# Performance work log

Hardware: AMD Instinct MI355X
Metric: run time of the kernel (lower is better)

The kernel has to match this reference:

```python
import jax, jax.numpy as jnp
import numpy as np

N_NODES = 20000
N_EDGES = 640000
IN_DIM = 256
HID = 128
N_GRAPHS = 64


def setup_inputs() -> dict:
    key = jax.random.key(0)
    ks = jax.random.split(key, 9)
    x = jax.random.normal(ks[0], (N_NODES, IN_DIM), jnp.float32)
    edge_index = jax.random.randint(ks[1], (2, N_EDGES), 0, N_NODES, dtype=jnp.int32)
    batch = jnp.sort(jax.random.randint(ks[2], (N_NODES,), 0, N_GRAPHS, dtype=jnp.int32))

    def lin(k, fan_in, fan_out):
        # torch.nn.Linear default init: U(-1/sqrt(fan_in), 1/sqrt(fan_in))
        bound = 1.0 / np.sqrt(fan_in)
        kw, kb = jax.random.split(k)
        W = jax.random.uniform(kw, (fan_in, fan_out), jnp.float32, -bound, bound)
        b = jax.random.uniform(kb, (fan_out,), jnp.float32, -bound, bound)
        return W, b

    W0, b0 = lin(ks[3], IN_DIM, HID)
    W1, b1 = lin(ks[4], HID, HID)
    W2, b2 = lin(ks[5], HID, HID)
    return dict(x=x, edge_index=edge_index, batch=batch,
                W0=W0, b0=b0, W1=W1, b1=b1, W2=W2, b2=b2)


def reference(x, edge_index, batch, W0, b0, W1, b1, W2, b2):
    src, dst = edge_index[0], edge_index[1]
    edge_batch = batch[src]  # [E] segment id per edge
    ones = jnp.ones((edge_batch.shape[0], 1), x.dtype)
    counts = jax.ops.segment_sum(ones, edge_batch, num_segments=N_GRAPHS)
    inv_counts = 1.0 / jnp.maximum(counts, 1.0)

    def pool(z):
        # gather endpoint features, concat -> [E, 2*HID], mean pool by graph
        edge_emb = jnp.concatenate([z[src], z[dst]], axis=1)
        return jax.ops.segment_sum(edge_emb, edge_batch, num_segments=N_GRAPHS) * inv_counts

    g = []
    z = x
    for W, b in ((W0, b0), (W1, b1), (W2, b2)):
        z = z @ W + b
        g.append(pool(z))
    return jnp.concatenate(g, axis=1)  # [N_GRAPHS, 3 * 2 * HID]
```

## Files before the change

### kernel.cpp

```cpp
#include <hip/hip_runtime.h>

#define N_NODES 20000
#define N_EDGES 640000
#define N_GRAPHS 64

#define NCHUNK 128
#define CHUNK_SZ 157
#define GSPLIT 8
#define GSUB 8

#define BG_TILE 2048
#define NBG 313
#define SEGCAP 80
#define GR_CAP 768
#define NSLOT4 (NBG * SEGCAP / 4)

#define CD_OFF      0
#define DEG_OFF     1280000
#define CNT_OFF     1300000
#define Y_OFF       1300064
#define PART_OFF    1316448
#define BH_OFF      3413600
#define VALS_OFF    3433632

__global__ __launch_bounds__(512) void bucket_g_k(const int* __restrict__ ei,
                                                  const int* __restrict__ batch,
                                                  unsigned* __restrict__ vals,
                                                  unsigned* __restrict__ bh,
                                                  float* __restrict__ Y) {
    __shared__ unsigned hist[N_GRAPHS];
    __shared__ unsigned base[N_GRAPHS + 1];
    __shared__ unsigned lv[BG_TILE];
    __shared__ unsigned char gidx[BG_TILE];
    const int t = threadIdx.x;
    const int blk = blockIdx.x;
    if (t < N_GRAPHS) hist[t] = 0u;
    __syncthreads();

    const int e0 = blk * BG_TILE;
    const int ecnt = (e0 + BG_TILE <= N_EDGES) ? BG_TILE : (N_EDGES - e0);
    unsigned pv[4], rnk[4], gg[4];
#pragma unroll
    for (int k = 0; k < 4; ++k) {
        int i = t + k * 512;
        if (i < ecnt) {
            unsigned s = (unsigned)ei[e0 + i];
            unsigned d = (unsigned)ei[N_EDGES + e0 + i];
            unsigned g = (unsigned)batch[s];
            pv[k] = (s << 15) | d;
            gg[k] = g;
            rnk[k] = atomicAdd(&hist[g], 1u);
        } else {
            gg[k] = 0xFFFFFFFFu;
        }
    }
    __syncthreads();
    if (t < N_GRAPHS) {
        unsigned v = hist[t];
        unsigned sum = v;
#pragma unroll
        for (int off = 1; off < 64; off <<= 1) {
            unsigned u = __shfl_up(sum, off, 64);
            if (t >= off) sum += u;
        }
        base[t + 1] = sum;
        if (t == 0) base[0] = 0u;
        bh[blk * N_GRAPHS + t] = (v > SEGCAP) ? SEGCAP : v;
    }
    __syncthreads();
    if (t < N_GRAPHS) {
        unsigned b0 = base[t], b1 = base[t + 1];
        for (unsigned i = b0; i < b1; ++i) gidx[i] = (unsigned char)t;
    }
#pragma unroll
    for (int k = 0; k < 4; ++k) {
        if (gg[k] != 0xFFFFFFFFu) lv[base[gg[k]] + rnk[k]] = pv[k];
    }
    __syncthreads();
    for (int i = t; i < ecnt; i += 512) {
        unsigned g = gidx[i];
        unsigned slot = (unsigned)i - base[g];
        if (slot < SEGCAP)
            vals[((size_t)g * NBG + blk) * SEGCAP + slot] = lv[i];
    }
    if (blk == 0) {
        float4* y4 = (float4*)Y;
        for (int i = t; i < 64 * 64; i += 512) y4[i] = make_float4(0.f, 0.f, 0.f, 0.f);
    }
}

__global__ __launch_bounds__(1024) void cd_col_k(const unsigned* __restrict__ vals,
                                                 const unsigned* __restrict__ bh,
                                                 const int* __restrict__ batch,
                                                 float* __restrict__ Cdcol,
                                                 float* __restrict__ deg,
                                                 float* __restrict__ counts) {
    __shared__ unsigned scnt[NBG];
    __shared__ unsigned dh[10000];
    __shared__ unsigned sdeg[GR_CAP];
    __shared__ int s_lo, s_hi;
    const int t = threadIdx.x;
    const int g = blockIdx.x;

    for (int i = t; i < 10000; i += 1024) dh[i] = 0u;
    if (t < NBG) scnt[t] = bh[t * N_GRAPHS + g];
    if (t < GR_CAP) sdeg[t] = 0u;
    if (t == 0) {
        int lo = 0, hi = N_NODES;
        while (lo < hi) { int m = (lo + hi) >> 1; if (batch[m] < g) lo = m + 1; else hi = m; }
        s_lo = lo;
        int lo2 = lo; hi = N_NODES;
        while (lo2 < hi) { int m = (lo2 + hi) >> 1; if (batch[m] < g + 1) lo2 = m + 1; else hi = m; }
        s_hi = lo2;
    }
    __syncthreads();
    const int lo = s_lo;

    const uint4* v4 = (const uint4*)(vals + (size_t)g * NBG * SEGCAP);
    for (int i = t; i < NSLOT4; i += 1024) {
        uint4 v = *(v4 + i);
        unsigned w = (unsigned)i * 4u;
        unsigned seg = (unsigned)(((unsigned long long)w * 53687092ull) >> 32);
        unsigned local = w - seg * 80u;
        unsigned c = scnt[seg];
#define CD_ONE(VX, L)                                                            \
        if ((L) < c) {                                                           \
            unsigned rd_ = (VX) & 0x7FFFu;                                       \
            atomicAdd(&dh[rd_ >> 1], 1u << ((rd_ & 1) * 16));                    \
            int rs_ = (int)((VX) >> 15) - lo;                                    \
            if ((unsigned)rs_ < (unsigned)GR_CAP) atomicAdd(&sdeg[rs_], 1u);     \
        }
        CD_ONE(v.x, local + 0u)
        CD_ONE(v.y, local + 1u)
        CD_ONE(v.z, local + 2u)
        CD_ONE(v.w, local + 3u)
#undef CD_ONE
    }
    __syncthreads();

    float2* outc = (float2*)(Cdcol + (size_t)g * N_NODES);
    for (int w = t; w < 10000; w += 1024) {
        unsigned v = dh[w];
        outc[w] = make_float2((float)(v & 0xFFFFu), (float)(v >> 16));
    }
    {
        const int range = s_hi - lo;
        for (int i = t; i < range; i += 1024) deg[lo + i] = (float)sdeg[i];
        if (t == 0) {
            unsigned tot = 0;
            for (int i = 0; i < NBG; ++i) tot += scnt[i];
            counts[g] = (float)tot;
        }
    }
}

#define FMA8(C0, C1, XV)                                          \
    acc[0].x = fmaf(C0.x, XV.x, acc[0].x); acc[0].y = fmaf(C0.x, XV.y, acc[0].y); \
    acc[0].z = fmaf(C0.x, XV.z, acc[0].z); acc[0].w = fmaf(C0.x, XV.w, acc[0].w); \
    acc[1].x = fmaf(C0.y, XV.x, acc[1].x); acc[1].y = fmaf(C0.y, XV.y, acc[1].y); \
    acc[1].z = fmaf(C0.y, XV.z, acc[1].z); acc[1].w = fmaf(C0.y, XV.w, acc[1].w); \
    acc[2].x = fmaf(C0.z, XV.x, acc[2].x); acc[2].y = fmaf(C0.z, XV.y, acc[2].y); \
    acc[2].z = fmaf(C0.z, XV.z, acc[2].z); acc[2].w = fmaf(C0.z, XV.w, acc[2].w); \
    acc[3].x = fmaf(C0.w, XV.x, acc[3].x); acc[3].y = fmaf(C0.w, XV.y, acc[3].y); \
    acc[3].z = fmaf(C0.w, XV.z, acc[3].z); acc[3].w = fmaf(C0.w, XV.w, acc[3].w); \
    acc[4].x = fmaf(C1.x, XV.x, acc[4].x); acc[4].y = fmaf(C1.x, XV.y, acc[4].y); \
    acc[4].z = fmaf(C1.x, XV.z, acc[4].z); acc[4].w = fmaf(C1.x, XV.w, acc[4].w); \
    acc[5].x = fmaf(C1.y, XV.x, acc[5].x); acc[5].y = fmaf(C1.y, XV.y, acc[5].y); \
    acc[5].z = fmaf(C1.y, XV.z, acc[5].z); acc[5].w = fmaf(C1.y, XV.w, acc[5].w); \
    acc[6].x = fmaf(C1.z, XV.x, acc[6].x); acc[6].y = fmaf(C1.z, XV.y, acc[6].y); \
    acc[6].z = fmaf(C1.z, XV.z, acc[6].z); acc[6].w = fmaf(C1.z, XV.w, acc[6].w); \
    acc[7].x = fmaf(C1.w, XV.x, acc[7].x); acc[7].y = fmaf(C1.w, XV.y, acc[7].y); \
    acc[7].z = fmaf(C1.w, XV.z, acc[7].z); acc[7].w = fmaf(C1.w, XV.w, acc[7].w);

__global__ __launch_bounds__(256) void pool_k(const float* __restrict__ x,
                                              const int* __restrict__ batch,
                                              const float* __restrict__ Cdcol,
                                              const float* __restrict__ deg,
                                              float* __restrict__ Y,
                                              float* __restrict__ part) {
    __shared__ float4 sc4[CHUNK_SZ * 2];
    __shared__ float sdeg[CHUNK_SZ];
    __shared__ int   sbatch[CHUNK_SZ];
    __shared__ float4 red[2 * GSUB * 64];

    const int t = threadIdx.x;
    const int fg = t & 63;
    const int p  = t >> 6;
    const int b = blockIdx.x & 127;
    const int j = blockIdx.x >> 7;
    const int n0 = b * CHUNK_SZ;
    const int cnt = (n0 + CHUNK_SZ <= N_NODES) ? CHUNK_SZ : (N_NODES - n0);

    float* sc = (float*)sc4;
    const float* cbase = Cdcol + (size_t)(j * GSUB) * N_NODES + n0;
#pragma unroll
    for (int k = 0; k < GSUB; ++k)
        for (int i = t; i < cnt; i += 256)
            sc[i * GSUB + k] = cbase[(size_t)k * N_NODES + i];
    if (j == 0) {
        for (int i = t; i < cnt; i += 256) {
            sdeg[i] = deg[n0 + i];
            sbatch[i] = batch[n0 + i];
        }
    }
    __syncthreads();

    const float4* xp = (const float4*)x + (size_t)n0 * 64 + fg;
#define XL(I) xp[(size_t)(I) * 64]
    float4 acc[GSUB];
#pragma unroll
    for (int k = 0; k < GSUB; ++k) acc[k] = make_float4(0.f, 0.f, 0.f, 0.f);

    if (j == 0) {
        float4 accs = make_float4(0.f, 0.f, 0.f, 0.f);
        int gprev = (p < cnt) ? sbatch[p] : 0;
        int i = p;
        float4 xn = make_float4(0.f, 0.f, 0.f, 0.f);
        if (i < cnt) xn = XL(i);
        for (; i < cnt; i += 4) {
            float4 xv = xn;
            if (i + 4 < cnt) xn = XL(i + 4);
            int g = sbatch[i];
            if (g != gprev) {
                float* yr = Y + gprev * 256 + fg * 4;
                atomicAdd(yr + 0, accs.x); atomicAdd(yr + 1, accs.y);
                atomicAdd(yr + 2, accs.z); atomicAdd(yr + 3, accs.w);
                accs = make_float4(0.f, 0.f, 0.f, 0.f);
                gprev = g;
            }
            float dg = sdeg[i];
            accs.x = fmaf(dg, xv.x, accs.x); accs.y = fmaf(dg, xv.y, accs.y);
            accs.z = fmaf(dg, xv.z, accs.z); accs.w = fmaf(dg, xv.w, accs.w);
            float4 c0 = sc4[i * 2], c1 = sc4[i * 2 + 1];
            FMA8(c0, c1, xv)
        }
        if (p < cnt) {
            float* yr = Y + gprev * 256 + fg * 4;
            atomicAdd(yr + 0, accs.x); atomicAdd(yr + 1, accs.y);
            atomicAdd(yr + 2, accs.z); atomicAdd(yr + 3, accs.w);
        }
    } else {
        int i = p;
        float4 xa, xb, xc, xd;
        if (i      < cnt) xa = XL(i);
        if (i + 4  < cnt) xb = XL(i + 4);
        if (i + 8  < cnt) xc = XL(i + 8);
        if (i + 12 < cnt) xd = XL(i + 12);
        for (; i + 12 < cnt; i += 16) {
            float4 y0 = xa, y1 = xb, y2 = xc, y3 = xd;
            if (i + 16 < cnt) xa = XL(i + 16);
            if (i + 20 < cnt) xb = XL(i + 20);
            if (i + 24 < cnt) xc = XL(i + 24);
            if (i + 28 < cnt) xd = XL(i + 28);
            {
                float4 c0 = sc4[i * 2], c1 = sc4[i * 2 + 1];
                FMA8(c0, c1, y0)
            }
            {
                float4 c0 = sc4[(i + 4) * 2], c1 = sc4[(i + 4) * 2 + 1];
                FMA8(c0, c1, y1)
            }
            {
                float4 c0 = sc4[(i + 8) * 2], c1 = sc4[(i + 8) * 2 + 1];
                FMA8(c0, c1, y2)
            }
            {
                float4 c0 = sc4[(i + 12) * 2], c1 = sc4[(i + 12) * 2 + 1];
                FMA8(c0, c1, y3)
            }
        }
        for (; i < cnt; i += 4) {
            float4 xv = XL(i);
            float4 c0 = sc4[i * 2], c1 = sc4[i * 2 + 1];
            FMA8(c0, c1, xv)
        }
    }
#undef XL

    if (p >= 2) {
#pragma unroll
        for (int k = 0; k < GSUB; ++k) red[(p - 2) * (GSUB * 64) + k * 64 + fg] = acc[k];
    }
    __syncthreads();
    if (p < 2) {
#pragma unroll
        for (int k = 0; k < GSUB; ++k) {
            float4 v = red[p * (GSUB * 64) + k * 64 + fg];
            acc[k].x += v.x; acc[k].y += v.y; acc[k].z += v.z; acc[k].w += v.w;
        }
    }
    __syncthreads();
    if (p == 1) {
#pragma unroll
        for (int k = 0; k < GSUB; ++k) red[k * 64 + fg] = acc[k];
    }
    __syncthreads();
    if (p == 0) {
        float4* part4 = (float4*)part;
#pragma unroll
        for (int k = 0; k < GSUB; ++k) {
            float4 v = red[k * 64 + fg];
            acc[k].x += v.x; acc[k].y += v.y; acc[k].z += v.z; acc[k].w += v.w;
            part4[(size_t)(b * 64 + j * GSUB + k) * 64 + fg] = acc[k];
        }
    }
}

__global__ __launch_bounds__(256) void chain2_k(const float* __restrict__ Y,
                                                const float* __restrict__ part,
                                                const float* __restrict__ counts,
                                                const float* __restrict__ W0, const float* __restrict__ b0,
                                                const float* __restrict__ W1, const float* __restrict__ b1,
                                                const float* __restrict__ W2, const float* __restrict__ b2,
                                                float* __restrict__ out) {
    __shared__ float m[256];
    __shared__ float pp[256];
    __shared__ float h[128];
    const int r = blockIdx.x;
    const int t = threadIdx.x;
    const int g = r & 63;
    const int half = (r >= 64) ? 128 : 0;
    const int tt = t & 127;
    const int ks = t >> 7;

    float c = counts[g];
    float inv = 1.0f / fmaxf(c, 1.0f);
    float beta = c * inv;

    if (r < 64) {
        m[t] = Y[g * 256 + t] * inv;
    } else {
        float s = 0.0f;
#pragma unroll 8
        for (int bb = 0; bb < NCHUNK; ++bb) s += part[(size_t)(bb * 64 + g) * 256 + t];
        m[t] = s * inv;
    }
    __syncthreads();

    {
        float s = 0.0f;
        const float* w = W0 + (ks * 128) * 128 + tt;
        const float* mm = m + ks * 128;
#pragma unroll 8
        for (int k = 0; k < 128; ++k) s = fmaf(mm[k], w[k * 128], s);
        pp[t] = s;
    }
    __syncthreads();
    if (t < 128) {
        float s1 = pp[t] + pp[t + 128] + beta * b0[t];
        out[g * 768 + 0 + half + t] = s1;
        h[t] = s1;
    }
    __syncthreads();

    {
        float s = 0.0f;
        const float* w = W1 + (ks * 64) * 128 + tt;
        const float* hh = h + ks * 64;
#pragma unroll 8
        for (int k = 0; k < 64; ++k) s = fmaf(hh[k], w[k * 128], s);
        pp[t] = s;
    }
    __syncthreads();
    float s2 = 0.0f;
    if (t < 128) {
        s2 = pp[t] + pp[t + 128] + beta * b1[t];
        out[g * 768 + 256 + half + t] = s2;
    }
    __syncthreads();
    if (t < 128) h[t] = s2;
    __syncthreads();

    {
        float s = 0.0f;
        const float* w = W2 + (ks * 64) * 128 + tt;
        const float* hh = h + ks * 64;
#pragma unroll 8
        for (int k = 0; k < 64; ++k) s = fmaf(hh[k], w[k * 128], s);
        pp[t] = s;
    }
    __syncthreads();
    if (t < 128) {
        float s3 = pp[t] + pp[t + 128] + beta * b2[t];
        out[g * 768 + 512 + half + t] = s3;
    }
}

extern "C" void kernel_launch(void* const* d_in, const int* in_sizes, int n_in,
                              void* d_out, int out_size, void* d_ws, size_t ws_size,
                              hipStream_t stream) {
    const float* x     = (const float*)d_in[0];
    const int*   ei    = (const int*)d_in[1];
    const int*   batch = (const int*)d_in[2];
    const float* W0    = (const float*)d_in[3];
    const float* b0    = (const float*)d_in[4];
    const float* W1    = (const float*)d_in[5];
    const float* b1    = (const float*)d_in[6];
    const float* W2    = (const float*)d_in[7];
    const float* b2    = (const float*)d_in[8];
    float* out = (float*)d_out;

    float*    ws     = (float*)d_ws;
    float*    Cdcol  = ws + CD_OFF;
    float*    deg    = ws + DEG_OFF;
    float*    counts = ws + CNT_OFF;
    float*    Y      = ws + Y_OFF;
    float*    part   = ws + PART_OFF;
    unsigned* bh     = (unsigned*)(ws + BH_OFF);
    unsigned* vals   = (unsigned*)(ws + VALS_OFF);

    bucket_g_k<<<NBG, 512, 0, stream>>>(ei, batch, vals, bh, Y);
    cd_col_k<<<N_GRAPHS, 1024, 0, stream>>>(vals, bh, batch, Cdcol, deg, counts);
    pool_k<<<NCHUNK * GSPLIT, 256, 0, stream>>>(x, batch, Cdcol, deg, Y, part);
    chain2_k<<<128, 256, 0, stream>>>(Y, part, counts, W0, b0, W1, b1, W2, b2, out);
}
```

Baseline: 123.1 us.

## Fuse four pipeline kernels into one cooperative persistent kernel with grid syncs

After: 323.7 us. 163% more time.

```diff
diff --git a/kernel.cpp b/kernel.cpp
--- a/kernel.cpp
+++ b/kernel.cpp
@@ -1,4 +1,7 @@
 #include <hip/hip_runtime.h>
+#include <hip/hip_cooperative_groups.h>
+
+namespace cg = cooperative_groups;
 
 #define N_NODES 20000
 #define N_EDGES 640000
@@ -8,127 +11,144 @@
 #define CHUNK_SZ 157
 #define GSPLIT 8
 #define GSUB 8
-
-#define BG_TILE 2048
-#define NBG 313
-#define SEGCAP 80
+#define NPOOL (NCHUNK * GSPLIT)
+
+#define BG_TILE 1024
+#define NBG 625
+#define SEGCAP 48
 #define GR_CAP 768
 #define NSLOT4 (NBG * SEGCAP / 4)
 
-#define CD_OFF      0
-#define DEG_OFF     1280000
-#define CNT_OFF     1300000
-#define Y_OFF       1300064
-#define PART_OFF    1316448
-#define BH_OFF      3413600
-#define VALS_OFF    3433632
-
-__global__ __launch_bounds__(512) void bucket_g_k(const int* __restrict__ ei,
-                                                  const int* __restrict__ batch,
-                                                  unsigned* __restrict__ vals,
-                                                  unsigned* __restrict__ bh,
-                                                  float* __restrict__ Y) {
-    __shared__ unsigned hist[N_GRAPHS];
-    __shared__ unsigned base[N_GRAPHS + 1];
-    __shared__ unsigned lv[BG_TILE];
-    __shared__ unsigned char gidx[BG_TILE];
+#define CD_OFF   0
+#define DEG_OFF  1280000
+#define CNT_OFF  1300000
+#define Y_OFF    1300064
+#define GLO_OFF  1316448
+#define PART_OFF 1316528
+#define BH_OFF   3413680
+#define VALS_OFF 3453680
+
+union ShU {
+    struct {
+        unsigned hist[N_GRAPHS];
+        unsigned base[N_GRAPHS + 1];
+        unsigned lv[BG_TILE];
+        unsigned char gidx[BG_TILE];
+    } bk;
+    struct {
+        unsigned dh[5000];
+        unsigned sdeg[GR_CAP];
+        unsigned rcnt[4];
+    } cd;
+    struct {
+        float4 sc4[CHUNK_SZ * 2];
+        float sdeg[CHUNK_SZ];
+        int sbatch[CHUNK_SZ];
+        float4 red[2 * GSUB * 64];
+    } pl;
+    struct {
+        float m[256];
+        float pp[256];
+        float h[128];
+    } ch;
+};
+
+__device__ __forceinline__ void phase_bucket(ShU& sh, int vb,
+        const int* __restrict__ ei, const int* __restrict__ batch, float* ws) {
+    unsigned* vals = (unsigned*)(ws + VALS_OFF);
+    unsigned* bh   = (unsigned*)(ws + BH_OFF);
     const int t = threadIdx.x;
-    const int blk = blockIdx.x;
-    if (t < N_GRAPHS) hist[t] = 0u;
-    __syncthreads();
-
-    const int e0 = blk * BG_TILE;
-    const int ecnt = (e0 + BG_TILE <= N_EDGES) ? BG_TILE : (N_EDGES - e0);
+    if (t < N_GRAPHS) sh.bk.hist[t] = 0u;
+    __syncthreads();
+    const int e0 = vb * BG_TILE;
     unsigned pv[4], rnk[4], gg[4];
 #pragma unroll
     for (int k = 0; k < 4; ++k) {
-        int i = t + k * 512;
-        if (i < ecnt) {
-            unsigned s = (unsigned)ei[e0 + i];
-            unsigned d = (unsigned)ei[N_EDGES + e0 + i];
-            unsigned g = (unsigned)batch[s];
-            pv[k] = (s << 15) | d;
-            gg[k] = g;
-            rnk[k] = atomicAdd(&hist[g], 1u);
-        } else {
-            gg[k] = 0xFFFFFFFFu;
-        }
+        int i = t + k * 256;
+        unsigned s = (unsigned)ei[e0 + i];
+        unsigned d = (unsigned)ei[N_EDGES + e0 + i];
+        unsigned g = (unsigned)batch[s];
+        pv[k] = (s << 15) | d;
+        gg[k] = g;
+        rnk[k] = atomicAdd(&sh.bk.hist[g], 1u);
     }
     __syncthreads();
     if (t < N_GRAPHS) {
-        unsigned v = hist[t];
+        unsigned v = sh.bk.hist[t];
         unsigned sum = v;
 #pragma unroll
         for (int off = 1; off < 64; off <<= 1) {
             unsigned u = __shfl_up(sum, off, 64);
             if (t >= off) sum += u;
         }
-        base[t + 1] = sum;
-        if (t == 0) base[0] = 0u;
-        bh[blk * N_GRAPHS + t] = (v > SEGCAP) ? SEGCAP : v;
+        sh.bk.base[t + 1] = sum;
+        if (t == 0) sh.bk.base[0] = 0u;
+        bh[vb * N_GRAPHS + t] = (v > SEGCAP) ? SEGCAP : v;
     }
     __syncthreads();
     if (t < N_GRAPHS) {
-        unsigned b0 = base[t], b1 = base[t + 1];
-        for (unsigned i = b0; i < b1; ++i) gidx[i] = (unsigned char)t;
-    }
-#pragma unroll
-    for (int k = 0; k < 4; ++k) {
-        if (gg[k] != 0xFFFFFFFFu) lv[base[gg[k]] + rnk[k]] = pv[k];
-    }
-    __syncthreads();
-    for (int i = t; i < ecnt; i += 512) {
-        unsigned g = gidx[i];
-        unsigned slot = (unsigned)i - base[g];
+        unsigned b0_ = sh.bk.base[t], b1_ = sh.bk.base[t + 1];
+        for (unsigned i = b0_; i < b1_; ++i) sh.bk.gidx[i] = (unsigned char)t;
+    }
+#pragma unroll
+    for (int k = 0; k < 4; ++k)
+        sh.bk.lv[sh.bk.base[gg[k]] + rnk[k]] = pv[k];
+    __syncthreads();
+    for (int i = t; i < BG_TILE; i += 256) {
+        unsigned g = sh.bk.gidx[i];
+        unsigned slot = (unsigned)i - sh.bk.base[g];
         if (slot < SEGCAP)
-            vals[((size_t)g * NBG + blk) * SEGCAP + slot] = lv[i];
-    }
-    if (blk == 0) {
-        float4* y4 = (float4*)Y;
-        for (int i = t; i < 64 * 64; i += 512) y4[i] = make_float4(0.f, 0.f, 0.f, 0.f);
-    }
-}
-
-__global__ __launch_bounds__(1024) void cd_col_k(const unsigned* __restrict__ vals,
-                                                 const unsigned* __restrict__ bh,
-                                                 const int* __restrict__ batch,
-                                                 float* __restrict__ Cdcol,
-                                                 float* __restrict__ deg,
-                                                 float* __restrict__ counts) {
-    __shared__ unsigned scnt[NBG];
-    __shared__ unsigned dh[10000];
-    __shared__ unsigned sdeg[GR_CAP];
-    __shared__ int s_lo, s_hi;
+            vals[((size_t)g * NBG + vb) * SEGCAP + slot] = sh.bk.lv[i];
+    }
+    __syncthreads();
+}
+
+__device__ __forceinline__ void phase_init(int bid, const int* __restrict__ batch, float* ws) {
     const int t = threadIdx.x;
-    const int g = blockIdx.x;
-
-    for (int i = t; i < 10000; i += 1024) dh[i] = 0u;
-    if (t < NBG) scnt[t] = bh[t * N_GRAPHS + g];
-    if (t < GR_CAP) sdeg[t] = 0u;
-    if (t == 0) {
-        int lo = 0, hi = N_NODES;
-        while (lo < hi) { int m = (lo + hi) >> 1; if (batch[m] < g) lo = m + 1; else hi = m; }
-        s_lo = lo;
-        int lo2 = lo; hi = N_NODES;
-        while (lo2 < hi) { int m = (lo2 + hi) >> 1; if (batch[m] < g + 1) lo2 = m + 1; else hi = m; }
-        s_hi = lo2;
-    }
-    __syncthreads();
-    const int lo = s_lo;
-
+    if (bid == 0) {
+        float4* y4 = (float4*)(ws + Y_OFF);
+        for (int i = t; i < 64 * 64; i += 256) y4[i] = make_float4(0.f, 0.f, 0.f, 0.f);
+    } else if (bid == 1) {
+        if (t <= N_GRAPHS) {
+            int lo = 0, hi = N_NODES;
+            while (lo < hi) { int m = (lo + hi) >> 1; if (batch[m] < t) lo = m + 1; else hi = m; }
+            ((unsigned*)(ws + GLO_OFF))[t] = (unsigned)lo;
+        }
+    }
+}
+
+__device__ __forceinline__ void phase_cd(ShU& sh, int vb, float* ws) {
+    const unsigned* vals = (const unsigned*)(ws + VALS_OFF);
+    const unsigned* bh   = (const unsigned*)(ws + BH_OFF);
+    const unsigned* glo  = (const unsigned*)(ws + GLO_OFF);
+    float* Cdcol  = ws + CD_OFF;
+    float* deg    = ws + DEG_OFF;
+    float* counts = ws + CNT_OFF;
+    const int t = threadIdx.x;
+    const int g = vb >> 1, h = vb & 1;
+    for (int i = t; i < 5000; i += 256) sh.cd.dh[i] = 0u;
+    if (h == 0) for (int i = t; i < GR_CAP; i += 256) sh.cd.sdeg[i] = 0u;
+    __syncthreads();
+    const int lo = (int)glo[g];
+    const int hi = (int)glo[g + 1];
+    const int dbase = h * 10000;
     const uint4* v4 = (const uint4*)(vals + (size_t)g * NBG * SEGCAP);
-    for (int i = t; i < NSLOT4; i += 1024) {
+    const unsigned* bhg = bh + g;
+    for (int i = t; i < NSLOT4; i += 256) {
         uint4 v = *(v4 + i);
         unsigned w = (unsigned)i * 4u;
-        unsigned seg = (unsigned)(((unsigned long long)w * 53687092ull) >> 32);
-        unsigned local = w - seg * 80u;
-        unsigned c = scnt[seg];
+        unsigned seg = w / 48u;
+        unsigned local = w - seg * 48u;
+        unsigned c = bhg[(size_t)seg * N_GRAPHS];
 #define CD_ONE(VX, L)                                                            \
         if ((L) < c) {                                                           \
-            unsigned rd_ = (VX) & 0x7FFFu;                                       \
-            atomicAdd(&dh[rd_ >> 1], 1u << ((rd_ & 1) * 16));                    \
-            int rs_ = (int)((VX) >> 15) - lo;                                    \
-            if ((unsigned)rs_ < (unsigned)GR_CAP) atomicAdd(&sdeg[rs_], 1u);     \
+            int rd_ = (int)((VX) & 0x7FFFu) - dbase;                             \
+            if ((unsigned)rd_ < 10000u)                                          \
+                atomicAdd(&sh.cd.dh[rd_ >> 1], 1u << ((rd_ & 1) * 16));          \
+            if (h == 0) {                                                        \
+                int rs_ = (int)((VX) >> 15) - lo;                                \
+                if ((unsigned)rs_ < (unsigned)GR_CAP) atomicAdd(&sh.cd.sdeg[rs_], 1u); \
+            }                                                                    \
         }
         CD_ONE(v.x, local + 0u)
         CD_ONE(v.y, local + 1u)
@@ -137,21 +157,23 @@
 #undef CD_ONE
     }
     __syncthreads();
-
-    float2* outc = (float2*)(Cdcol + (size_t)g * N_NODES);
-    for (int w = t; w < 10000; w += 1024) {
-        unsigned v = dh[w];
-        outc[w] = make_float2((float)(v & 0xFFFFu), (float)(v >> 16));
-    }
-    {
-        const int range = s_hi - lo;
-        for (int i = t; i < range; i += 1024) deg[lo + i] = (float)sdeg[i];
-        if (t == 0) {
-            unsigned tot = 0;
-            for (int i = 0; i < NBG; ++i) tot += scnt[i];
-            counts[g] = (float)tot;
-        }
-    }
+    float2* outc = (float2*)(Cdcol + (size_t)g * N_NODES + dbase);
+    for (int wd = t; wd < 5000; wd += 256) {
+        unsigned v = sh.cd.dh[wd];
+        outc[wd] = make_float2((float)(v & 0xFFFFu), (float)(v >> 16));
+    }
+    if (h == 0) {
+        const int range = hi - lo;
+        for (int i = t; i < range; i += 256) deg[lo + i] = (float)sh.cd.sdeg[i];
+        unsigned s = 0;
+        for (int seg = t; seg < NBG; seg += 256) s += bhg[(size_t)seg * N_GRAPHS];
+#pragma unroll
+        for (int off = 32; off; off >>= 1) s += __shfl_down(s, off, 64);
+        if ((t & 63) == 0) sh.cd.rcnt[t >> 6] = s;
+        __syncthreads();
+        if (t == 0) counts[g] = (float)(sh.cd.rcnt[0] + sh.cd.rcnt[1] + sh.cd.rcnt[2] + sh.cd.rcnt[3]);
+    }
+    __syncthreads();
 }
 
 #define FMA8(C0, C1, XV)                                          \
@@ -172,26 +194,21 @@
     acc[7].x = fmaf(C1.w, XV.x, acc[7].x); acc[7].y = fmaf(C1.w, XV.y, acc[7].y); \
     acc[7].z = fmaf(C1.w, XV.z, acc[7].z); acc[7].w = fmaf(C1.w, XV.w, acc[7].w);
 
-__global__ __launch_bounds__(256) void pool_k(const float* __restrict__ x,
-                                              const int* __restrict__ batch,
-                                              const float* __restrict__ Cdcol,
-                                              const float* __restrict__ deg,
-                                              float* __restrict__ Y,
-                                              float* __restrict__ part) {
-    __shared__ float4 sc4[CHUNK_SZ * 2];
-    __shared__ float sdeg[CHUNK_SZ];
-    __shared__ int   sbatch[CHUNK_SZ];
-    __shared__ float4 red[2 * GSUB * 64];
-
+__device__ __forceinline__ void phase_pool(ShU& sh, int vb,
+        const float* __restrict__ x, const int* __restrict__ batch, float* ws) {
+    const float* Cdcol = ws + CD_OFF;
+    const float* deg   = ws + DEG_OFF;
+    float* Y    = ws + Y_OFF;
+    float* part = ws + PART_OFF;
     const int t = threadIdx.x;
     const int fg = t & 63;
     const int p  = t >> 6;
-    const int b = blockIdx.x & 127;
-    const int j = blockIdx.x >> 7;
+    const int b = vb & 127;
+    const int j = vb >> 7;
     const int n0 = b * CHUNK_SZ;
     const int cnt = (n0 + CHUNK_SZ <= N_NODES) ? CHUNK_SZ : (N_NODES - n0);
 
-    float* sc = (float*)sc4;
+    float* sc = (float*)sh.pl.sc4;
     const float* cbase = Cdcol + (size_t)(j * GSUB) * N_NODES + n0;
 #pragma unroll
     for (int k = 0; k < GSUB; ++k)
@@ -199,8 +216,8 @@
             sc[i * GSUB + k] = cbase[(size_t)k * N_NODES + i];
     if (j == 0) {
         for (int i = t; i < cnt; i += 256) {
-            sdeg[i] = deg[n0 + i];
-            sbatch[i] = batch[n0 + i];
+            sh.pl.sdeg[i] = deg[n0 + i];
+            sh.pl.sbatch[i] = batch[n0 + i];
         }
     }
     __syncthreads();
@@ -213,14 +230,14 @@
 
     if (j == 0) {
         float4 accs = make_float4(0.f, 0.f, 0.f, 0.f);
-        int gprev = (p < cnt) ? sbatch[p] : 0;
+        int gprev = (p < cnt) ? sh.pl.sbatch[p] : 0;
         int i = p;
         float4 xn = make_float4(0.f, 0.f, 0.f, 0.f);
         if (i < cnt) xn = XL(i);
         for (; i < cnt; i += 4) {
             float4 xv = xn;
             if (i + 4 < cnt) xn = XL(i + 4);
-            int g = sbatch[i];
+            int g = sh.pl.sbatch[i];
             if (g != gprev) {
                 float* yr = Y + gprev * 256 + fg * 4;
                 atomicAdd(yr + 0, accs.x); atomicAdd(yr + 1, accs.y);
@@ -228,10 +245,10 @@
                 accs = make_float4(0.f, 0.f, 0.f, 0.f);
                 gprev = g;
             }
-            float dg = sdeg[i];
+            float dg = sh.pl.sdeg[i];
             accs.x = fmaf(dg, xv.x, accs.x); accs.y = fmaf(dg, xv.y, accs.y);
             accs.z = fmaf(dg, xv.z, accs.z); accs.w = fmaf(dg, xv.w, accs.w);
-            float4 c0 = sc4[i * 2], c1 = sc4[i * 2 + 1];
+            float4 c0 = sh.pl.sc4[i * 2], c1 = sh.pl.sc4[i * 2 + 1];
             FMA8(c0, c1, xv)
         }
         if (p < cnt) {
@@ -252,26 +269,14 @@
             if (i + 20 < cnt) xb = XL(i + 20);
             if (i + 24 < cnt) xc = XL(i + 24);
             if (i + 28 < cnt) xd = XL(i + 28);
-            {
-                float4 c0 = sc4[i * 2], c1 = sc4[i * 2 + 1];
-                FMA8(c0, c1, y0)
-            }
-            {
-                float4 c0 = sc4[(i + 4) * 2], c1 = sc4[(i + 4) * 2 + 1];
-                FMA8(c0, c1, y1)
-            }
-            {
-                float4 c0 = sc4[(i + 8) * 2], c1 = sc4[(i + 8) * 2 + 1];
-                FMA8(c0, c1, y2)
-            }
-            {
-                float4 c0 = sc4[(i + 12) * 2], c1 = sc4[(i + 12) * 2 + 1];
-                FMA8(c0, c1, y3)
-            }
+            { float4 c0 = sh.pl.sc4[i * 2],       c1 = sh.pl.sc4[i * 2 + 1];       FMA8(c0, c1, y0) }
+            { float4 c0 = sh.pl.sc4[(i + 4) * 2], c1 = sh.pl.sc4[(i + 4) * 2 + 1]; FMA8(c0, c1, y1) }
+            { float4 c0 = sh.pl.sc4[(i + 8) * 2], c1 = sh.pl.sc4[(i + 8) * 2 + 1]; FMA8(c0, c1, y2) }
+            { float4 c0 = sh.pl.sc4[(i + 12) * 2],c1 = sh.pl.sc4[(i + 12) * 2 + 1];FMA8(c0, c1, y3) }
         }
         for (; i < cnt; i += 4) {
             float4 xv = XL(i);
-            float4 c0 = sc4[i * 2], c1 = sc4[i * 2 + 1];
+            float4 c0 = sh.pl.sc4[i * 2], c1 = sh.pl.sc4[i * 2 + 1];
             FMA8(c0, c1, xv)
         }
     }
@@ -279,44 +284,43 @@
 
     if (p >= 2) {
 #pragma unroll
-        for (int k = 0; k < GSUB; ++k) red[(p - 2) * (GSUB * 64) + k * 64 + fg] = acc[k];
+        for (int k = 0; k < GSUB; ++k) sh.pl.red[(p - 2) * (GSUB * 64) + k * 64 + fg] = acc[k];
     }
     __syncthreads();
     if (p < 2) {
 #pragma unroll
         for (int k = 0; k < GSUB; ++k) {
-            float4 v = red[p * (GSUB * 64) + k * 64 + fg];
+            float4 v = sh.pl.red[p * (GSUB * 64) + k * 64 + fg];
             acc[k].x += v.x; acc[k].y += v.y; acc[k].z += v.z; acc[k].w += v.w;
         }
     }
     __syncthreads();
     if (p == 1) {
 #pragma unroll
-        for (int k = 0; k < GSUB; ++k) red[k * 64 + fg] = acc[k];
+        for (int k = 0; k < GSUB; ++k) sh.pl.red[k * 64 + fg] = acc[k];
     }
     __syncthreads();
     if (p == 0) {
         float4* part4 = (float4*)part;
 #pragma unroll
         for (int k = 0; k < GSUB; ++k) {
-            float4 v = red[k * 64 + fg];
+            float4 v = sh.pl.red[k * 64 + fg];
             acc[k].x += v.x; acc[k].y += v.y; acc[k].z += v.z; acc[k].w += v.w;
             part4[(size_t)(b * 64 + j * GSUB + k) * 64 + fg] = acc[k];
         }
     }
-}
-
-__global__ __launch_bounds__(256) void chain2_k(const float* __restrict__ Y,
-                                                const float* __restrict__ part,
-                                                const float* __restrict__ counts,
-                                                const float* __restrict__ W0, const float* __restrict__ b0,
-                                                const float* __restrict__ W1, const float* __restrict__ b1,
-                                                const float* __restrict__ W2, const float* __restrict__ b2,
-                                                float* __restrict__ out) {
-    __shared__ float m[256];
-    __shared__ float pp[256];
-    __shared__ float h[128];
-    const int r = blockIdx.x;
+    __syncthreads();
+}
+
+__device__ __forceinline__ void phase_chain(ShU& sh, int vb, float* ws,
+        const float* __restrict__ W0, const float* __restrict__ b0,
+        const float* __restrict__ W1, const float* __restrict__ b1,
+        const float* __restrict__ W2, const float* __restrict__ b2,
+        float* __restrict__ out) {
+    const float* Y      = ws + Y_OFF;
+    const float* part   = ws + PART_OFF;
+    const float* counts = ws + CNT_OFF;
+    const int r = vb;
     const int t = threadIdx.x;
     const int g = r & 63;
     const int half = (r >= 64) ? 128 : 0;
@@ -328,62 +332,109 @@
     float beta = c * inv;
 
     if (r < 64) {
-        m[t] = Y[g * 256 + t] * inv;
+        sh.ch.m[t] = Y[g * 256 + t] * inv;
     } else {
         float s = 0.0f;
 #pragma unroll 8
         for (int bb = 0; bb < NCHUNK; ++bb) s += part[(size_t)(bb * 64 + g) * 256 + t];
-        m[t] = s * inv;
+        sh.ch.m[t] = s * inv;
     }
     __syncthreads();
 
     {
         float s = 0.0f;
         const float* w = W0 + (ks * 128) * 128 + tt;
-        const float* mm = m + ks * 128;
+        const float* mm = sh.ch.m + ks * 128;
 #pragma unroll 8
         for (int k = 0; k < 128; ++k) s = fmaf(mm[k], w[k * 128], s);
-        pp[t] = s;
+        sh.ch.pp[t] = s;
     }
     __syncthreads();
     if (t < 128) {
-        float s1 = pp[t] + pp[t + 128] + beta * b0[t];
+        float s1 = sh.ch.pp[t] + sh.ch.pp[t + 128] + beta * b0[t];
         out[g * 768 + 0 + half + t] = s1;
-        h[t] = s1;
+        sh.ch.h[t] = s1;
     }
     __syncthreads();
 
     {
         float s = 0.0f;
         const float* w = W1 + (ks * 64) * 128 + tt;
-        const float* hh = h + ks * 64;
+        const float* hh = sh.ch.h + ks * 64;
 #pragma unroll 8
         for (int k = 0; k < 64; ++k) s = fmaf(hh[k], w[k * 128], s);
-        pp[t] = s;
+        sh.ch.pp[t] = s;
     }
     __syncthreads();
     float s2 = 0.0f;
     if (t < 128) {
-        s2 = pp[t] + pp[t + 128] + beta * b1[t];
+        s2 = sh.ch.pp[t] + sh.ch.pp[t + 128] + beta * b1[t];
         out[g * 768 + 256 + half + t] = s2;
     }
     __syncthreads();
-    if (t < 128) h[t] = s2;
+    if (t < 128) sh.ch.h[t] = s2;
     __syncthreads();
 
     {
         float s = 0.0f;
         const float* w = W2 + (ks * 64) * 128 + tt;
-        const float* hh = h + ks * 64;
+        const float* hh = sh.ch.h + ks * 64;
 #pragma unroll 8
         for (int k = 0; k < 64; ++k) s = fmaf(hh[k], w[k * 128], s);
-        pp[t] = s;
+        sh.ch.pp[t] = s;
     }
     __syncthreads();
     if (t < 128) {
-        float s3 = pp[t] + pp[t + 128] + beta * b2[t];
+        float s3 = sh.ch.pp[t] + sh.ch.pp[t + 128] + beta * b2[t];
         out[g * 768 + 512 + half + t] = s3;
     }
+    __syncthreads();
+}
+
+__global__ __launch_bounds__(256, 4) void fused_k(
+        const float* __restrict__ x, const int* __restrict__ ei, const int* __restrict__ batch,
+        const float* __restrict__ W0, const float* __restrict__ b0,
+        const float* __restrict__ W1, const float* __restrict__ b1,
+        const float* __restrict__ W2, const float* __restrict__ b2,
+        float* __restrict__ out, float* ws) {
+    __shared__ ShU sh;
+    cg::grid_group grid = cg::this_grid();
+    for (int vb = blockIdx.x; vb < NBG; vb += gridDim.x)
+        phase_bucket(sh, vb, ei, batch, ws);
+    phase_init(blockIdx.x, batch, ws);
+    grid.sync();
+    for (int vb = blockIdx.x; vb < 2 * N_GRAPHS; vb += gridDim.x)
+        phase_cd(sh, vb, ws);
+    grid.sync();
+    for (int vb = blockIdx.x; vb < NPOOL; vb += gridDim.x)
+        phase_pool(sh, vb, x, batch, ws);
+    grid.sync();
+    for (int vb = blockIdx.x; vb < 128; vb += gridDim.x)
+        phase_chain(sh, vb, ws, W0, b0, W1, b1, W2, b2, out);
+}
+
+__global__ __launch_bounds__(256) void p1_k(const int* __restrict__ ei,
+                                            const int* __restrict__ batch, float* ws) {
+    __shared__ ShU sh;
+    phase_bucket(sh, blockIdx.x, ei, batch, ws);
+    phase_init(blockIdx.x, batch, ws);
+}
+__global__ __launch_bounds__(256) void p2_k(float* ws) {
+    __shared__ ShU sh;
+    phase_cd(sh, blockIdx.x, ws);
+}
+__global__ __launch_bounds__(256) void p3_k(const float* __restrict__ x,
+                                            const int* __restrict__ batch, float* ws) {
+    __shared__ ShU sh;
+    phase_pool(sh, blockIdx.x, x, batch, ws);
+}
+__global__ __launch_bounds__(256) void p4_k(float* ws,
+        const float* __restrict__ W0, const float* __restrict__ b0,
+        const float* __restrict__ W1, const float* __restrict__ b1,
+        const float* __restrict__ W2, const float* __restrict__ b2,
+        float* __restrict__ out) {
+    __shared__ ShU sh;
+    phase_chain(sh, blockIdx.x, ws, W0, b0, W1, b1, W2, b2, out);
 }
 
 extern "C" void kernel_launch(void* const* d_in, const int* in_sizes, int n_in,
@@ -399,18 +450,24 @@
     const float* W2    = (const float*)d_in[7];
     const float* b2    = (const float*)d_in[8];
     float* out = (float*)d_out;
-
-    float*    ws     = (float*)d_ws;
-    float*    Cdcol  = ws + CD_OFF;
-    float*    deg    = ws + DEG_OFF;
-    float*    counts = ws + CNT_OFF;
-    float*    Y      = ws + Y_OFF;
-    float*    part   = ws + PART_OFF;
-    unsigned* bh     = (unsigned*)(ws + BH_OFF);
-    unsigned* vals   = (unsigned*)(ws + VALS_OFF);
-
-    bucket_g_k<<<NBG, 512, 0, stream>>>(ei, batch, vals, bh, Y);
-    cd_col_k<<<N_GRAPHS, 1024, 0, stream>>>(vals, bh, batch, Cdcol, deg, counts);
-    pool_k<<<NCHUNK * GSPLIT, 256, 0, stream>>>(x, batch, Cdcol, deg, Y, part);
-    chain2_k<<<128, 256, 0, stream>>>(Y, part, counts, W0, b0, W1, b1, W2, b2, out);
-}
+    float* ws  = (float*)d_ws;
+
+    void* kargs[] = {(void*)&x, (void*)&ei, (void*)&batch,
+                     (void*)&W0, (void*)&b0, (void*)&W1, (void*)&b1, (void*)&W2, (void*)&b2,
+                     (void*)&out, (void*)&ws};
+
+    int nb = 0;
+    hipError_t qerr = hipOccupancyMaxActiveBlocksPerMultiprocessor(&nb, (const void*)fused_k, 256, 0);
+    hipError_t lerr = hipErrorUnknown;
+    if (qerr == hipSuccess && nb > 0) {
+        int grid = nb * 256;
+        if (grid > 1024) grid = 1024;
+        lerr = hipLaunchCooperativeKernel((void*)fused_k, dim3(grid), dim3(256), kargs, 0, stream);
+    }
+    if (lerr != hipSuccess) {
+        p1_k<<<NBG, 256, 0, stream>>>(ei, batch, ws);
+        p2_k<<<2 * N_GRAPHS, 256, 0, stream>>>(ws);
+        p3_k<<<NPOOL, 256, 0, stream>>>(x, batch, ws);
+        p4_k<<<128, 256, 0, stream>>>(ws, W0, b0, W1, b1, W2, b2, out);
+    }
+}
```

## Restructure pool kernel: one block per node chunk, warps split by graph group

Applied to the files above, without the earlier changes.

Measured after the change: 145.7 us. 18.4% more time.

```diff
diff --git a/kernel.cpp b/kernel.cpp
--- a/kernel.cpp
+++ b/kernel.cpp
@@ -4,9 +4,8 @@
 #define N_EDGES 640000
 #define N_GRAPHS 64
 
-#define NCHUNK 128
-#define CHUNK_SZ 157
-#define GSPLIT 8
+#define NCHUNK 250
+#define CHUNK_SZ 80
 #define GSUB 8
 
 #define BG_TILE 2048
@@ -15,13 +14,13 @@
 #define GR_CAP 768
 #define NSLOT4 (NBG * SEGCAP / 4)
 
-#define CD_OFF      0
-#define DEG_OFF     1280000
-#define CNT_OFF     1300000
-#define Y_OFF       1300064
-#define PART_OFF    1316448
-#define BH_OFF      3413600
-#define VALS_OFF    3433632
+#define CD_OFF   0
+#define DEG_OFF  1280000
+#define CNT_OFF  1300000
+#define Y_OFF    1300064
+#define PART_OFF 1316448
+#define BH_OFF   5412448
+#define VALS_OFF 5432480
 
 __global__ __launch_bounds__(512) void bucket_g_k(const int* __restrict__ ei,
                                                   const int* __restrict__ batch,
@@ -69,8 +68,8 @@
     }
     __syncthreads();
     if (t < N_GRAPHS) {
-        unsigned b0 = base[t], b1 = base[t + 1];
-        for (unsigned i = b0; i < b1; ++i) gidx[i] = (unsigned char)t;
+        unsigned b0_ = base[t], b1_ = base[t + 1];
+        for (unsigned i = b0_; i < b1_; ++i) gidx[i] = (unsigned char)t;
     }
 #pragma unroll
     for (int k = 0; k < 4; ++k) {
@@ -172,138 +171,76 @@
     acc[7].x = fmaf(C1.w, XV.x, acc[7].x); acc[7].y = fmaf(C1.w, XV.y, acc[7].y); \
     acc[7].z = fmaf(C1.w, XV.z, acc[7].z); acc[7].w = fmaf(C1.w, XV.w, acc[7].w);
 
-__global__ __launch_bounds__(256) void pool_k(const float* __restrict__ x,
+__global__ __launch_bounds__(512) void pool_k(const float* __restrict__ x,
                                               const int* __restrict__ batch,
                                               const float* __restrict__ Cdcol,
                                               const float* __restrict__ deg,
                                               float* __restrict__ Y,
                                               float* __restrict__ part) {
-    __shared__ float4 sc4[CHUNK_SZ * 2];
+    __shared__ float4 sc4[CHUNK_SZ * 17];
     __shared__ float sdeg[CHUNK_SZ];
     __shared__ int   sbatch[CHUNK_SZ];
-    __shared__ float4 red[2 * GSUB * 64];
 
     const int t = threadIdx.x;
     const int fg = t & 63;
     const int p  = t >> 6;
-    const int b = blockIdx.x & 127;
-    const int j = blockIdx.x >> 7;
+    const int b  = blockIdx.x;
     const int n0 = b * CHUNK_SZ;
-    const int cnt = (n0 + CHUNK_SZ <= N_NODES) ? CHUNK_SZ : (N_NODES - n0);
-
-    float* sc = (float*)sc4;
-    const float* cbase = Cdcol + (size_t)(j * GSUB) * N_NODES + n0;
-#pragma unroll
-    for (int k = 0; k < GSUB; ++k)
-        for (int i = t; i < cnt; i += 256)
-            sc[i * GSUB + k] = cbase[(size_t)k * N_NODES + i];
-    if (j == 0) {
-        for (int i = t; i < cnt; i += 256) {
-            sdeg[i] = deg[n0 + i];
-            sbatch[i] = batch[n0 + i];
-        }
+
+    float* scf = (float*)sc4;
+    for (int e = t; e < N_GRAPHS * CHUNK_SZ; e += 512) {
+        unsigned g = (unsigned)e / (unsigned)CHUNK_SZ;
+        unsigned i = (unsigned)e - g * (unsigned)CHUNK_SZ;
+        scf[i * 68u + g] = Cdcol[(size_t)g * N_NODES + n0 + i];
+    }
+    if (t < CHUNK_SZ) {
+        sdeg[t] = deg[n0 + t];
+        sbatch[t] = batch[n0 + t];
     }
     __syncthreads();
 
     const float4* xp = (const float4*)x + (size_t)n0 * 64 + fg;
-#define XL(I) xp[(size_t)(I) * 64]
     float4 acc[GSUB];
 #pragma unroll
     for (int k = 0; k < GSUB; ++k) acc[k] = make_float4(0.f, 0.f, 0.f, 0.f);
-
-    if (j == 0) {
-        float4 accs = make_float4(0.f, 0.f, 0.f, 0.f);
-        int gprev = (p < cnt) ? sbatch[p] : 0;
-        int i = p;
-        float4 xn = make_float4(0.f, 0.f, 0.f, 0.f);
-        if (i < cnt) xn = XL(i);
-        for (; i < cnt; i += 4) {
-            float4 xv = xn;
-            if (i + 4 < cnt) xn = XL(i + 4);
-            int g = sbatch[i];
+    float4 accs = make_float4(0.f, 0.f, 0.f, 0.f);
+    int gprev = -1;
+
+    float4 xn0 = xp[0];
+    float4 xn1 = xp[64];
+    for (int i = 0; i < CHUNK_SZ; ++i) {
+        float4 xv = xn0;
+        xn0 = xn1;
+        if (i + 2 < CHUNK_SZ) xn1 = xp[(size_t)(i + 2) * 64];
+        float4 c0 = sc4[i * 17 + 2 * p];
+        float4 c1 = sc4[i * 17 + 2 * p + 1];
+        int g = sbatch[i];
+        if ((g >> 3) == p) {
             if (g != gprev) {
-                float* yr = Y + gprev * 256 + fg * 4;
-                atomicAdd(yr + 0, accs.x); atomicAdd(yr + 1, accs.y);
-                atomicAdd(yr + 2, accs.z); atomicAdd(yr + 3, accs.w);
+                if (gprev >= 0) {
+                    float* yr = Y + gprev * 256 + fg * 4;
+                    atomicAdd(yr + 0, accs.x); atomicAdd(yr + 1, accs.y);
+                    atomicAdd(yr + 2, accs.z); atomicAdd(yr + 3, accs.w);
+                }
                 accs = make_float4(0.f, 0.f, 0.f, 0.f);
                 gprev = g;
             }
             float dg = sdeg[i];
             accs.x = fmaf(dg, xv.x, accs.x); accs.y = fmaf(dg, xv.y, accs.y);
             accs.z = fmaf(dg, xv.z, accs.z); accs.w = fmaf(dg, xv.w, accs.w);
-            float4 c0 = sc4[i * 2], c1 = sc4[i * 2 + 1];
-            FMA8(c0, c1, xv)
-        }
-        if (p < cnt) {
-            float* yr = Y + gprev * 256 + fg * 4;
-            atomicAdd(yr + 0, accs.x); atomicAdd(yr + 1, accs.y);
-            atomicAdd(yr + 2, accs.z); atomicAdd(yr + 3, accs.w);
-        }
-    } else {
-        int i = p;
-        float4 xa, xb, xc, xd;
-        if (i      < cnt) xa = XL(i);
-        if (i + 4  < cnt) xb = XL(i + 4);
-        if (i + 8  < cnt) xc = XL(i + 8);
-        if (i + 12 < cnt) xd = XL(i + 12);
-        for (; i + 12 < cnt; i += 16) {
-            float4 y0 = xa, y1 = xb, y2 = xc, y3 = xd;
-            if (i + 16 < cnt) xa = XL(i + 16);
-            if (i + 20 < cnt) xb = XL(i + 20);
-            if (i + 24 < cnt) xc = XL(i + 24);
-            if (i + 28 < cnt) xd = XL(i + 28);
-            {
-                float4 c0 = sc4[i * 2], c1 = sc4[i * 2 + 1];
-                FMA8(c0, c1, y0)
-            }
-            {
-                float4 c0 = sc4[(i + 4) * 2], c1 = sc4[(i + 4) * 2 + 1];
-                FMA8(c0, c1, y1)
-            }
-            {
-                float4 c0 = sc4[(i + 8) * 2], c1 = sc4[(i + 8) * 2 + 1];
-                FMA8(c0, c1, y2)
-            }
-            {
-                float4 c0 = sc4[(i + 12) * 2], c1 = sc4[(i + 12) * 2 + 1];
-                FMA8(c0, c1, y3)
-            }
-        }
-        for (; i < cnt; i += 4) {
-            float4 xv = XL(i);
-            float4 c0 = sc4[i * 2], c1 = sc4[i * 2 + 1];
-            FMA8(c0, c1, xv)
-        }
-    }
-#undef XL
-
-    if (p >= 2) {
-#pragma unroll
-        for (int k = 0; k < GSUB; ++k) red[(p - 2) * (GSUB * 64) + k * 64 + fg] = acc[k];
-    }
-    __syncthreads();
-    if (p < 2) {
-#pragma unroll
-        for (int k = 0; k < GSUB; ++k) {
-            float4 v = red[p * (GSUB * 64) + k * 64 + fg];
-            acc[k].x += v.x; acc[k].y += v.y; acc[k].z += v.z; acc[k].w += v.w;
-        }
-    }
-    __syncthreads();
-    if (p == 1) {
-#pragma unroll
-        for (int k = 0; k < GSUB; ++k) red[k * 64 + fg] = acc[k];
-    }
-    __syncthreads();
-    if (p == 0) {
-        float4* part4 = (float4*)part;
-#pragma unroll
-        for (int k = 0; k < GSUB; ++k) {
-            float4 v = red[k * 64 + fg];
-            acc[k].x += v.x; acc[k].y += v.y; acc[k].z += v.z; acc[k].w += v.w;
-            part4[(size_t)(b * 64 + j * GSUB + k) * 64 + fg] = acc[k];
-        }
-    }
+        }
+        FMA8(c0, c1, xv)
+    }
+    if (gprev >= 0) {
+        float* yr = Y + gprev * 256 + fg * 4;
+        atomicAdd(yr + 0, accs.x); atomicAdd(yr + 1, accs.y);
+        atomicAdd(yr + 2, accs.z); atomicAdd(yr + 3, accs.w);
+    }
+
+    float4* part4 = (float4*)part;
+#pragma unroll
+    for (int k = 0; k < GSUB; ++k)
+        part4[(size_t)(b * 64 + p * GSUB + k) * 64 + fg] = acc[k];
 }
 
 __global__ __launch_bounds__(256) void chain2_k(const float* __restrict__ Y,
@@ -331,7 +268,7 @@
         m[t] = Y[g * 256 + t] * inv;
     } else {
         float s = 0.0f;
-#pragma unroll 8
+#pragma unroll 5
         for (int bb = 0; bb < NCHUNK; ++bb) s += part[(size_t)(bb * 64 + g) * 256 + t];
         m[t] = s * inv;
     }
@@ -411,6 +348,6 @@
 
     bucket_g_k<<<NBG, 512, 0, stream>>>(ei, batch, vals, bh, Y);
     cd_col_k<<<N_GRAPHS, 1024, 0, stream>>>(vals, bh, batch, Cdcol, deg, counts);
-    pool_k<<<NCHUNK * GSPLIT, 256, 0, stream>>>(x, batch, Cdcol, deg, Y, part);
+    pool_k<<<NCHUNK, 512, 0, stream>>>(x, batch, Cdcol, deg, Y, part);
     chain2_k<<<128, 256, 0, stream>>>(Y, part, counts, W0, b0, W1, b1, W2, b2, out);
 }
```

## Split cd_col across two blocks per graph and precompute graph node bounds

Applied to the files above, without the earlier changes.

After: 120.0 us. 2.5% less time.

```diff
diff --git a/kernel.cpp b/kernel.cpp
--- a/kernel.cpp
+++ b/kernel.cpp
@@ -22,18 +22,32 @@
 #define PART_OFF    1316448
 #define BH_OFF      3413600
 #define VALS_OFF    3433632
+#define GLO_OFF     5036192
 
 __global__ __launch_bounds__(512) void bucket_g_k(const int* __restrict__ ei,
                                                   const int* __restrict__ batch,
                                                   unsigned* __restrict__ vals,
                                                   unsigned* __restrict__ bh,
-                                                  float* __restrict__ Y) {
+                                                  float* __restrict__ Y,
+                                                  unsigned* __restrict__ glo) {
     __shared__ unsigned hist[N_GRAPHS];
     __shared__ unsigned base[N_GRAPHS + 1];
     __shared__ unsigned lv[BG_TILE];
     __shared__ unsigned char gidx[BG_TILE];
     const int t = threadIdx.x;
     const int blk = blockIdx.x;
+
+    if (blk == NBG) {
+        if (t < N_GRAPHS + 1) {
+            int lo = 0, hi = N_NODES;
+            while (lo < hi) { int m = (lo + hi) >> 1; if (batch[m] < t) lo = m + 1; else hi = m; }
+            glo[t] = (unsigned)lo;
+        }
+        float4* y4 = (float4*)Y;
+        for (int i = t; i < 64 * 64; i += 512) y4[i] = make_float4(0.f, 0.f, 0.f, 0.f);
+        return;
+    }
+
     if (t < N_GRAPHS) hist[t] = 0u;
     __syncthreads();
 
@@ -69,8 +83,8 @@
     }
     __syncthreads();
     if (t < N_GRAPHS) {
-        unsigned b0 = base[t], b1 = base[t + 1];
-        for (unsigned i = b0; i < b1; ++i) gidx[i] = (unsigned char)t;
+        unsigned b0_ = base[t], b1_ = base[t + 1];
+        for (unsigned i = b0_; i < b1_; ++i) gidx[i] = (unsigned char)t;
     }
 #pragma unroll
     for (int k = 0; k < 4; ++k) {
@@ -83,38 +97,29 @@
         if (slot < SEGCAP)
             vals[((size_t)g * NBG + blk) * SEGCAP + slot] = lv[i];
     }
-    if (blk == 0) {
-        float4* y4 = (float4*)Y;
-        for (int i = t; i < 64 * 64; i += 512) y4[i] = make_float4(0.f, 0.f, 0.f, 0.f);
-    }
 }
 
 __global__ __launch_bounds__(1024) void cd_col_k(const unsigned* __restrict__ vals,
                                                  const unsigned* __restrict__ bh,
-                                                 const int* __restrict__ batch,
+                                                 const unsigned* __restrict__ glo,
                                                  float* __restrict__ Cdcol,
                                                  float* __restrict__ deg,
                                                  float* __restrict__ counts) {
     __shared__ unsigned scnt[NBG];
-    __shared__ unsigned dh[10000];
+    __shared__ unsigned dh[5000];
     __shared__ unsigned sdeg[GR_CAP];
-    __shared__ int s_lo, s_hi;
+    __shared__ unsigned rc[16];
     const int t = threadIdx.x;
-    const int g = blockIdx.x;
-
-    for (int i = t; i < 10000; i += 1024) dh[i] = 0u;
+    const int g = blockIdx.x & 63;
+    const int h = blockIdx.x >> 6;
+    const int dbase = h * 10000;
+
+    for (int i = t; i < 5000; i += 1024) dh[i] = 0u;
+    if (h) { if (t < GR_CAP) sdeg[t] = 0u; }
     if (t < NBG) scnt[t] = bh[t * N_GRAPHS + g];
-    if (t < GR_CAP) sdeg[t] = 0u;
-    if (t == 0) {
-        int lo = 0, hi = N_NODES;
-        while (lo < hi) { int m = (lo + hi) >> 1; if (batch[m] < g) lo = m + 1; else hi = m; }
-        s_lo = lo;
-        int lo2 = lo; hi = N_NODES;
-        while (lo2 < hi) { int m = (lo2 + hi) >> 1; if (batch[m] < g + 1) lo2 = m + 1; else hi = m; }
-        s_hi = lo2;
-    }
-    __syncthreads();
-    const int lo = s_lo;
+    __syncthreads();
+    const int lo = (int)glo[g];
+    const int hi = (int)glo[g + 1];
 
     const uint4* v4 = (const uint4*)(vals + (size_t)g * NBG * SEGCAP);
     for (int i = t; i < NSLOT4; i += 1024) {
@@ -125,10 +130,13 @@
         unsigned c = scnt[seg];
 #define CD_ONE(VX, L)                                                            \
         if ((L) < c) {                                                           \
-            unsigned rd_ = (VX) & 0x7FFFu;                                       \
-            atomicAdd(&dh[rd_ >> 1], 1u << ((rd_ & 1) * 16));                    \
-            int rs_ = (int)((VX) >> 15) - lo;                                    \
-            if ((unsigned)rs_ < (unsigned)GR_CAP) atomicAdd(&sdeg[rs_], 1u);     \
+            int rd_ = (int)((VX) & 0x7FFFu) - dbase;                             \
+            if ((unsigned)rd_ < 10000u)                                          \
+                atomicAdd(&dh[rd_ >> 1], 1u << ((rd_ & 1) * 16));                \
+            if (h) {                                                             \
+                int rs_ = (int)((VX) >> 15) - lo;                                \
+                if ((unsigned)rs_ < (unsigned)GR_CAP) atomicAdd(&sdeg[rs_], 1u); \
+            }                                                                    \
         }
         CD_ONE(v.x, local + 0u)
         CD_ONE(v.y, local + 1u)
@@ -138,17 +146,25 @@
     }
     __syncthreads();
 
-    float2* outc = (float2*)(Cdcol + (size_t)g * N_NODES);
-    for (int w = t; w < 10000; w += 1024) {
+    float2* outc = (float2*)(Cdcol + (size_t)g * N_NODES + dbase);
+    for (int w = t; w < 5000; w += 1024) {
         unsigned v = dh[w];
         outc[w] = make_float2((float)(v & 0xFFFFu), (float)(v >> 16));
     }
-    {
-        const int range = s_hi - lo;
+    if (h) {
+        const int range = hi - lo;
         for (int i = t; i < range; i += 1024) deg[lo + i] = (float)sdeg[i];
+    } else {
+        unsigned s = 0;
+        for (int i = t; i < NBG; i += 1024) s += scnt[i];
+#pragma unroll
+        for (int off = 32; off; off >>= 1) s += __shfl_down(s, off, 64);
+        if ((t & 63) == 0) rc[t >> 6] = s;
+        __syncthreads();
         if (t == 0) {
             unsigned tot = 0;
-            for (int i = 0; i < NBG; ++i) tot += scnt[i];
+#pragma unroll
+            for (int i = 0; i < 16; ++i) tot += rc[i];
             counts[g] = (float)tot;
         }
     }
@@ -408,9 +424,10 @@
     float*    part   = ws + PART_OFF;
     unsigned* bh     = (unsigned*)(ws + BH_OFF);
     unsigned* vals   = (unsigned*)(ws + VALS_OFF);
-
-    bucket_g_k<<<NBG, 512, 0, stream>>>(ei, batch, vals, bh, Y);
-    cd_col_k<<<N_GRAPHS, 1024, 0, stream>>>(vals, bh, batch, Cdcol, deg, counts);
+    unsigned* glo    = (unsigned*)(ws + GLO_OFF);
+
+    bucket_g_k<<<NBG + 1, 512, 0, stream>>>(ei, batch, vals, bh, Y, glo);
+    cd_col_k<<<128, 1024, 0, stream>>>(vals, bh, glo, Cdcol, deg, counts);
     pool_k<<<NCHUNK * GSPLIT, 256, 0, stream>>>(x, batch, Cdcol, deg, Y, part);
     chain2_k<<<128, 256, 0, stream>>>(Y, part, counts, W0, b0, W1, b1, W2, b2, out);
 }
```
